# Optimization experiments

Hardware: AMD Instinct MI355X
Metric: run time of the kernel (lower is better)

## Reference

```python
import jax, jax.numpy as jnp
import numpy as np

B, S = 32, 128          # batch, seq_len
C, K = 256, 128         # num_concept, dim_k (== dim_e == dim_correct)
DC = 128                # dim_correct
NQ, NIT, NUT = 10000, 1024, 1024


def _xavier(k, shape):
    fan_out, fan_in = shape[0], shape[1]
    bound = float(np.sqrt(6.0 / (fan_in + fan_out)))
    return jax.random.uniform(k, shape, jnp.float32, -bound, bound)


def setup_inputs() -> dict:
    key = jax.random.key(0)
    ks = jax.random.split(key, 16)
    question_seq = jax.random.randint(ks[0], (B, S), 0, NQ + 1)
    interval_time_seq = jax.random.randint(ks[1], (B, S), 0, NIT + 1)
    use_time_seq = jax.random.randint(ks[2], (B, S), 0, NUT + 1)
    correct_seq = jnp.round(jax.random.uniform(ks[3], (B, S))).astype(jnp.float32)
    E_q = _xavier(ks[4], (NQ + 1, K))
    E_it = _xavier(ks[5], (NIT + 1, K))
    E_ut = _xavier(ks[6], (NUT + 1, K))
    q_matrix = (jax.random.uniform(ks[7], (NQ + 1, C)) < 0.03).astype(jnp.float32)
    h0 = _xavier(ks[8], (C, K))  # xavier init of the initial concept memory
    W1 = _xavier(ks[9], (K, K + K + DC)); b1 = jnp.zeros((K,), jnp.float32)
    W2 = _xavier(ks[10], (K, 4 * K));     b2 = jnp.zeros((K,), jnp.float32)
    W3 = _xavier(ks[11], (K, 4 * K));     b3 = jnp.zeros((K,), jnp.float32)
    W4 = _xavier(ks[12], (K, 3 * K));     b4 = jnp.zeros((K,), jnp.float32)
    W5 = _xavier(ks[13], (K, 2 * K));     b5 = jnp.zeros((K,), jnp.float32)
    return dict(question_seq=question_seq, interval_time_seq=interval_time_seq,
                use_time_seq=use_time_seq, correct_seq=correct_seq,
                E_q=E_q, E_it=E_it, E_ut=E_ut, q_matrix=q_matrix, h0=h0,
                W1=W1, b1=b1, W2=W2, b2=b2, W3=W3, b3=b3,
                W4=W4, b4=b4, W5=W5, b5=b5)


def _forward(question_seq, interval_time_seq, use_time_seq, correct_seq,
             E_q, E_it, E_ut, q_matrix, h0,
             W1, b1, W2, b2, W3, b3, W4, b4, W5, b5):
    bsz, slen = question_seq.shape
    dim_k = h0.shape[1]
    dim_c = W1.shape[1] - 2 * dim_k

    q_emb = E_q[question_seq]            # [B,S,K]
    it_emb = E_it[interval_time_seq]     # [B,S,K]
    ut_emb = E_ut[use_time_seq]          # [B,S,K]
    c_emb = jnp.broadcast_to(correct_seq[..., None], (bsz, slen, dim_c))
    all_learning = jnp.concatenate([q_emb, ut_emb, c_emb], -1) @ W1.T + b1  # [B,S,K]
    qe = q_matrix[question_seq]          # [B,S,C]

    h_pre0 = jnp.tile(h0[None], (bsz, 1, 1))                     # [B,C,K]
    h_tilde0 = jnp.einsum('bc,bck->bk', qe[:, 0], h_pre0)        # q_e @ h at t=0
    learning0 = jnp.zeros((bsz, dim_k), all_learning.dtype)

    # split linear_4 weight over its (h_pre, LG, it) concat blocks
    W4h, W4l, W4i = W4[:, :dim_k], W4[:, dim_k:2 * dim_k], W4[:, 2 * dim_k:]

    # time-major per-step inputs for t = 0 .. S-2
    xs = (jnp.swapaxes(it_emb[:, :-1], 0, 1),
          jnp.swapaxes(all_learning[:, :-1], 0, 1),
          jnp.swapaxes(qe[:, :-1], 0, 1),
          jnp.swapaxes(qe[:, 1:], 0, 1),
          jnp.swapaxes(q_emb[:, 1:], 0, 1))

    def step(carry, x):
        h_pre, h_tilde_pre, learning_pre = carry
        it, learning, qe_t, qe_n, qemb_n = x
        cat = jnp.concatenate([learning_pre, it, learning, h_tilde_pre], -1)  # [B,4K]
        learning_gain = jnp.tanh(cat @ W2.T + b2)
        gamma_l = jax.nn.sigmoid(cat @ W3.T + b3)
        LG = gamma_l * (learning_gain + 1.0) * 0.5                 # [B,K]
        LG_tilde = qe_t[:, :, None] * LG[:, None, :]               # [B,C,K] outer write
        gamma_f = jax.nn.sigmoid(jnp.einsum('bck,jk->bcj', h_pre, W4h)
                                 + (LG @ W4l.T + it @ W4i.T + b4)[:, None, :])
        h = LG_tilde + gamma_f * h_pre                             # [B,C,K]
        h_tilde = jnp.einsum('bc,bck->bk', qe_n, h)                # read for t+1
        y = jax.nn.sigmoid(jnp.concatenate([qemb_n, h_tilde], -1) @ W5.T + b5).sum(-1) / dim_k
        return (h, h_tilde, learning), y

    _, ys = jax.lax.scan(step, (h_pre0, h_tilde0, learning0), xs)  # ys: [S-1,B]
    pred = jnp.concatenate([jnp.zeros((bsz, 1), ys.dtype), ys.T], axis=1)
    return pred


def reference(question_seq, interval_time_seq, use_time_seq, correct_seq,
              E_q, E_it, E_ut, q_matrix, h0,
              W1, b1, W2, b2, W3, b3, W4, b4, W5, b5):
    return _forward(question_seq, interval_time_seq, use_time_seq, correct_seq,
                    E_q, E_it, E_ut, q_matrix, h0,
                    W1, b1, W2, b2, W3, b3, W4, b4, W5, b5)
```

## Files before the change

### kernel.cpp

```cpp
#include <hip/hip_runtime.h>
#include <hip/hip_bf16.h>


typedef __bf16 bf16x8 __attribute__((ext_vector_type(8)));
typedef __bf16 bf16x4 __attribute__((ext_vector_type(4)));
typedef float f32x4 __attribute__((ext_vector_type(4)));

#define HROW 136
#define HBUF (256*HROW)

__device__ __forceinline__ float sigmf(float x){
  return __builtin_amdgcn_rcpf(1.0f + __expf(-x));
}

__device__ __forceinline__ bf16x8 cvt8(float4 a, float4 b){
  bf16x8 r;
  r[0]=(__bf16)a.x; r[1]=(__bf16)a.y; r[2]=(__bf16)a.z; r[3]=(__bf16)a.w;
  r[4]=(__bf16)b.x; r[5]=(__bf16)b.y; r[6]=(__bf16)b.z; r[7]=(__bf16)b.w;
  return r;
}

__device__ __forceinline__ void mk_hilo(float4 a, float4 b, bf16x8& hi, bf16x8& lo){
  float v[8] = {a.x,a.y,a.z,a.w,b.x,b.y,b.z,b.w};
  #pragma unroll
  for (int i = 0; i < 8; i++){
    __bf16 h = (__bf16)v[i];
    hi[i] = h;
    lo[i] = (__bf16)(v[i] - (float)h);
  }
}

__device__ __forceinline__ f32x4 mfma16(bf16x8 a, bf16x8 b, f32x4 c){
  return __builtin_amdgcn_mfma_f32_16x16x32_bf16(a, b, c, 0, 0, 0);
}

__device__ __forceinline__ void red16(f32x4& r){
  #pragma unroll
  for (int m = 1; m < 16; m <<= 1){
    r[0] += __shfl_xor(r[0], m);
    r[1] += __shfl_xor(r[1], m);
    r[2] += __shfl_xor(r[2], m);
    r[3] += __shfl_xor(r[3], m);
  }
}

__global__ __launch_bounds__(256) void k1_al(
    const int* __restrict__ qseq, const int* __restrict__ utseq,
    const float* __restrict__ corr,
    const float* __restrict__ Eq, const float* __restrict__ Eut,
    const float* __restrict__ W1, const float* __restrict__ b1,
    const float* __restrict__ W5, const float* __restrict__ b5,
    float* __restrict__ AL, float* __restrict__ pre5)
{
  __shared__ __bf16 inA[64*256];
  __shared__ float corrs[64];
  __shared__ float b1s[128], b5s[128], rsp[256];
  const int tid = threadIdx.x, blk = blockIdx.x;
  if (tid < 128){ b1s[tid]=b1[tid]; b5s[tid]=b5[tid]; }
  {
    int j = tid & 127, hf = tid >> 7;
    const float* p = W1 + j*384 + 256 + hf*64;
    float s = 0.f;
    for (int i = 0; i < 64; i++) s += p[i];
    rsp[tid] = s;
  }
  {
    int r = tid >> 2, seg = tid & 3;
    int R = blk*64 + r;
    int qi = qseq[R], ui = utseq[R];
    if (seg == 0) corrs[r] = corr[R];
    for (int i = 0; i < 64; i++){
      int col = seg*64 + i;
      float v = (col < 128) ? Eq[qi*128 + col] : Eut[ui*128 + (col-128)];
      inA[((r*256 + col) ^ ((r&7)<<3))] = (__bf16)v;
    }
  }
  __syncthreads();
  const int w = tid >> 6, lane = tid & 63;
  const int la = lane & 15, g = lane >> 4;
  const int rbase = w*16;
  bf16x8 af[8];
  #pragma unroll
  for (int kt = 0; kt < 8; kt++){
    int idx = ((rbase+la)*256 + kt*32 + g*8) ^ ((la&7)<<3);
    af[kt] = *(const bf16x8*)&inA[idx];
  }
  for (int jt = 0; jt < 8; jt++){
    f32x4 acc = {0.f,0.f,0.f,0.f};
    const float* Wb = W1 + (jt*16+la)*384;
    #pragma unroll
    for (int kt = 0; kt < 8; kt++){
      const float* p = Wb + kt*32 + g*8;
      acc = mfma16(af[kt], cvt8(*(const float4*)p, *(const float4*)(p+4)), acc);
    }
    int j = jt*16 + la;
    float rsj = rsp[j] + rsp[j+128];
    #pragma unroll
    for (int rr = 0; rr < 4; rr++){
      int row = rbase + g*4 + rr;
      int R = blk*64 + row;
      AL[R*128 + j] = acc[rr] + b1s[j] + corrs[row]*rsj;
    }
  }
  for (int jt = 0; jt < 8; jt++){
    f32x4 acc = {0.f,0.f,0.f,0.f};
    const float* Wb = W5 + (jt*16+la)*256;
    #pragma unroll
    for (int kt = 0; kt < 4; kt++){
      const float* p = Wb + kt*32 + g*8;
      acc = mfma16(af[kt], cvt8(*(const float4*)p, *(const float4*)(p+4)), acc);
    }
    int j = jt*16 + la;
    #pragma unroll
    for (int rr = 0; rr < 4; rr++){
      int row = rbase + g*4 + rr;
      int R = blk*64 + row;
      pre5[R*128 + j] = acc[rr] + b5s[j];
    }
  }
}

__global__ __launch_bounds__(256) void k2_pre(
    const int* __restrict__ itseq, const float* __restrict__ Eit,
    const float* __restrict__ AL,
    const float* __restrict__ W2, const float* __restrict__ W3,
    const float* __restrict__ W4,
    const float* __restrict__ b2, const float* __restrict__ b3,
    const float* __restrict__ b4,
    float* __restrict__ pre23, float* __restrict__ pre4)
{
  __shared__ __bf16 inA[64*384];
  __shared__ int obase[64];
  __shared__ float b2s[128], b3s[128], b4s[128];
  const int tid = threadIdx.x, blk = blockIdx.x;
  if (tid < 128){ b2s[tid]=b2[tid]; b3s[tid]=b3[tid]; b4s[tid]=b4[tid]; }
  {
    int r = tid >> 2, seg = tid & 3;
    int R = blk*64 + r;
    bool valid = (R < 4064);
    int b_ = R / 127, tau = R % 127;
    if (seg == 0) obase[r] = valid ? (b_*127 + tau) : -1;
    int itv = valid ? itseq[b_*128 + tau] : 0;
    for (int i = 0; i < 96; i++){
      int col = seg*96 + i;
      float v = 0.f;
      if (valid){
        if (col < 128)      v = (tau > 0) ? AL[(b_*128 + tau-1)*128 + col] : 0.f;
        else if (col < 256) v = Eit[itv*128 + (col-128)];
        else                v = AL[(b_*128 + tau)*128 + (col-256)];
      }
      inA[((r*384 + col) ^ ((r&7)<<3))] = (__bf16)v;
    }
  }
  __syncthreads();
  const int w = tid >> 6, lane = tid & 63;
  const int la = lane & 15, g = lane >> 4;
  const int rbase = w*16;
  bf16x8 af[12];
  #pragma unroll
  for (int kt = 0; kt < 12; kt++){
    int idx = ((rbase+la)*384 + kt*32 + g*8) ^ ((la&7)<<3);
    af[kt] = *(const bf16x8*)&inA[idx];
  }
  for (int jt = 0; jt < 16; jt++){
    f32x4 acc = {0.f,0.f,0.f,0.f};
    int j = jt*16 + la;
    const float* Wb = (j < 128) ? (W2 + j*512) : (W3 + (j-128)*512);
    #pragma unroll
    for (int kt = 0; kt < 12; kt++){
      const float* p = Wb + kt*32 + g*8;
      acc = mfma16(af[kt], cvt8(*(const float4*)p, *(const float4*)(p+4)), acc);
    }
    float bias = (j < 128) ? b2s[j] : b3s[j-128];
    #pragma unroll
    for (int rr = 0; rr < 4; rr++){
      int row = rbase + g*4 + rr;
      int ob = obase[row];
      if (ob >= 0) pre23[ob*256 + j] = acc[rr] + bias;
    }
  }
  for (int jt = 0; jt < 8; jt++){
    f32x4 acc = {0.f,0.f,0.f,0.f};
    int j = jt*16 + la;
    const float* Wb = W4 + j*384 + 256;
    #pragma unroll
    for (int kk = 0; kk < 4; kk++){
      const float* p = Wb + kk*32 + g*8;
      acc = mfma16(af[4+kk], cvt8(*(const float4*)p, *(const float4*)(p+4)), acc);
    }
    #pragma unroll
    for (int rr = 0; rr < 4; rr++){
      int row = rbase + g*4 + rr;
      int ob = obase[row];
      if (ob >= 0) pre4[ob*128 + j] = acc[rr] + b4s[j];
    }
  }
}

#define SCAN_LDS_BYTES (37184*4)

__global__ __launch_bounds__(512, 2) void lpkt_scan(
    const float* __restrict__ qmat, const int* __restrict__ qseq,
    const float* __restrict__ h0,
    const float* __restrict__ W2, const float* __restrict__ W3,
    const float* __restrict__ W4,
    const float* __restrict__ pre23, const float* __restrict__ pre4,
    float* __restrict__ hist)
{
  extern __shared__ float lds[];
  __bf16* hB   = (__bf16*)lds;
  float*  htb0 = lds + 34816;
  float*  htb1 = lds + 35072;
  float*  LGb  = lds + 35328;
  __bf16* LGh  = (__bf16*)(lds + 35456);
  float*  qeb  = lds + 35520;
  float*  p23L = lds + 36288;
  float*  p4L  = lds + 36800;
  int*    qsl  = (int*)(lds + 37056);

  const int tid  = threadIdx.x;
  const int b    = blockIdx.x;
  const int lane = tid & 63;
  const int w    = tid >> 6;
  const int la   = lane & 15, g = lane >> 4;
  const int jq   = w & 3;
  const int ch   = w >> 2;

  bf16x8 af[2][4];
  bf16x8 af4l[2][4];
  #pragma unroll
  for (int jj = 0; jj < 2; jj++){
    #pragma unroll
    for (int kt = 0; kt < 4; kt++){
      const float* ph = W4 + ((jq*2+jj)*16+la)*384 + kt*32 + g*8;
      const float* pl = W4 + ((jq*2+jj)*16+la)*384 + 128 + kt*32 + g*8;
      af[jj][kt]   = cvt8(*(const float4*)ph, *(const float4*)(ph+4));
      af4l[jj][kt] = cvt8(*(const float4*)pl, *(const float4*)(pl+4));
    }
  }
  bf16x8 af23[2][4];
  #pragma unroll
  for (int kt = 0; kt < 4; kt++){
    const float* p2 = W2 + (w*16+la)*512 + 384 + kt*32 + g*8;
    const float* p3 = W3 + (w*16+la)*512 + 384 + kt*32 + g*8;
    af23[0][kt] = cvt8(*(const float4*)p2, *(const float4*)(p2+4));
    af23[1][kt] = cvt8(*(const float4*)p3, *(const float4*)(p3+4));
  }

  int rb[8], wb[8];
  #pragma unroll
  for (int cg = 0; cg < 8; cg++){
    const int c_ = ch*128 + cg*16 + la;
    rb[cg] = c_*HROW + g*8;
    wb[cg] = c_*HROW + jq*32 + g*4;
  }

  if (tid < 128) qsl[tid] = qseq[b*128 + tid];
  __syncthreads();
  const float* pre23b = pre23 + b*127*256;
  const float* pre4b  = pre4  + b*127*128;
  if (tid < 64)       *(float4*)&qeb[tid*4] = *(const float4*)(qmat + (size_t)qsl[0]*256 + tid*4);
  else if (tid < 128) *(float4*)&qeb[256 + (tid-64)*4] = *(const float4*)(qmat + (size_t)qsl[1]*256 + (tid-64)*4);
  else if (tid < 192) *(float4*)&p23L[(tid-128)*4] = *(const float4*)(pre23b + (tid-128)*4);
  else if (tid < 224) *(float4*)&p4L[(tid-192)*4]  = *(const float4*)(pre4b  + (tid-192)*4);

  float4 hreg[8][2];
  #pragma unroll
  for (int cg = 0; cg < 8; cg++){
    const int c_ = ch*128 + cg*16 + la;
    #pragma unroll
    for (int jj = 0; jj < 2; jj++){
      const int k0 = (jq*2+jj)*16 + g*4;
      float4 v = *(const float4*)(h0 + c_*128 + k0);
      hreg[cg][jj] = v;
      bf16x4 hb; hb[0]=(__bf16)v.x; hb[1]=(__bf16)v.y; hb[2]=(__bf16)v.z; hb[3]=(__bf16)v.w;
      *(bf16x4*)&hB[wb[cg] + jj*16] = hb;
    }
  }
  __syncthreads();
  {
    f32x4 r0 = {0.f,0.f,0.f,0.f}, r1 = {0.f,0.f,0.f,0.f};
    #pragma unroll
    for (int cg = 0; cg < 8; cg++){
      const int c_ = ch*128 + cg*16 + la;
      float q = qeb[c_];
      float4 h0v = hreg[cg][0], h1v = hreg[cg][1];
      r0[0] += q*h0v.x; r0[1] += q*h0v.y; r0[2] += q*h0v.z; r0[3] += q*h0v.w;
      r1[0] += q*h1v.x; r1[1] += q*h1v.y; r1[2] += q*h1v.z; r1[3] += q*h1v.w;
    }
    red16(r0); red16(r1);
    if (la == 0){
      float4 s0 = {r0[0],r0[1],r0[2],r0[3]};
      float4 s1 = {r1[0],r1[1],r1[2],r1[3]};
      *(float4*)&htb0[ch*128 + jq*32 + g*4]      = s0;
      *(float4*)&htb0[ch*128 + jq*32 + 16 + g*4] = s1;
    }
  }
  __syncthreads();

  int i0 = 0, i1 = 1, i2 = 2;

  for (int tau = 0; tau < 127; tau++){
    float* htc = (tau & 1) ? htb1 : htb0;
    float* htn = (tau & 1) ? htb0 : htb1;
    float* qec = qeb + i0*256;
    float* qen = qeb + i1*256;
    float* qep = qeb + i2*256;
    const float* p23c = p23L + (tau & 1)*256;
    const float* p4c  = p4L  + (tau & 1)*128;
    const int roff = (tau & 1) ? HBUF : 0;
    const int woff = (tau & 1) ? 0 : HBUF;

    {
      bf16x8 xh[4], xl[4];
      #pragma unroll
      for (int kt = 0; kt < 4; kt++){
        int k0 = kt*32 + g*8;
        float4 a0 = *(const float4*)&htc[k0];
        float4 a1 = *(const float4*)&htc[k0+4];
        float4 b0 = *(const float4*)&htc[128 + k0];
        float4 b1v = *(const float4*)&htc[128 + k0+4];
        a0.x += b0.x; a0.y += b0.y; a0.z += b0.z; a0.w += b0.w;
        a1.x += b1v.x; a1.y += b1v.y; a1.z += b1v.z; a1.w += b1v.w;
        mk_hilo(a0, a1, xh[kt], xl[kt]);
      }
      f32x4 aLh = {0.f,0.f,0.f,0.f}, aLl = {0.f,0.f,0.f,0.f};
      f32x4 aGh = {0.f,0.f,0.f,0.f}, aGl = {0.f,0.f,0.f,0.f};
      #pragma unroll
      for (int kt = 0; kt < 4; kt++){
        aLh = mfma16(af23[0][kt], xh[kt], aLh);
        aLl = mfma16(af23[0][kt], xl[kt], aLl);
        aGh = mfma16(af23[1][kt], xh[kt], aGh);
        aGl = mfma16(af23[1][kt], xl[kt], aGl);
      }
      float4 lp4 = *(const float4*)&p23c[w*16 + g*4];
      float4 gp4 = *(const float4*)&p23c[128 + w*16 + g*4];
      float4 LG4;
      LG4.x = sigmf(aGh[0]+aGl[0]+gp4.x) * sigmf(2.f*(aLh[0]+aLl[0]+lp4.x));
      LG4.y = sigmf(aGh[1]+aGl[1]+gp4.y) * sigmf(2.f*(aLh[1]+aLl[1]+lp4.y));
      LG4.z = sigmf(aGh[2]+aGl[2]+gp4.z) * sigmf(2.f*(aLh[2]+aLl[2]+lp4.z));
      LG4.w = sigmf(aGh[3]+aGl[3]+gp4.w) * sigmf(2.f*(aLh[3]+aLl[3]+lp4.w));
      if (la == 0){
        *(float4*)&LGb[w*16 + g*4] = LG4;
        bf16x4 lgp;
        lgp[0]=(__bf16)LG4.x; lgp[1]=(__bf16)LG4.y;
        lgp[2]=(__bf16)LG4.z; lgp[3]=(__bf16)LG4.w;
        *(bf16x4*)&LGh[w*16 + g*4] = lgp;
      }
    }
    __syncthreads();

    float4 pf23, pf4, pfqe;
    const bool dopf = (tau < 126);
    const bool do23 = dopf && (tid < 64);
    const bool do4  = dopf && (tid >= 64) && (tid < 96);
    const bool doqe = dopf && (tid >= 448);
    if (do23) pf23 = *(const float4*)(pre23b + (tau+1)*256 + tid*4);
    if (do4)  pf4  = *(const float4*)(pre4b  + (tau+1)*128 + (tid-64)*4);
    if (doqe) pfqe = *(const float4*)(qmat + (size_t)qsl[tau+2]*256 + (tid-448)*4);
    if (tau > 0 && tid >= 96 && tid < 128){
      int i = (tid - 96)*4;
      float4 v0 = *(const float4*)&htc[i];
      float4 v1 = *(const float4*)&htc[128 + i];
      float4 v = {v0.x+v1.x, v0.y+v1.y, v0.z+v1.z, v0.w+v1.w};
      *(float4*)(hist + ((size_t)b*127 + (tau-1))*128 + i) = v;
    }

    float4 z4[2];
    {
      bf16x8 lh[4];
      #pragma unroll
      for (int kt = 0; kt < 4; kt++)
        lh[kt] = *(const bf16x8*)&LGh[kt*32 + g*8];
      #pragma unroll
      for (int jj = 0; jj < 2; jj++){
        f32x4 az = {0.f,0.f,0.f,0.f};
        #pragma unroll
        for (int kt = 0; kt < 4; kt++)
          az = mfma16(af4l[jj][kt], lh[kt], az);
        float4 zp = *(const float4*)&p4c[(jq*2+jj)*16 + g*4];
        z4[jj].x = az[0]+zp.x; z4[jj].y = az[1]+zp.y;
        z4[jj].z = az[2]+zp.z; z4[jj].w = az[3]+zp.w;
      }
    }
    float4 lg4[2];
    #pragma unroll
    for (int jj = 0; jj < 2; jj++)
      lg4[jj] = *(const float4*)&LGb[(jq*2+jj)*16 + g*4];

    bf16x8 bA[4], bB[4];
    {
      const int base = rb[0] + roff;
      #pragma unroll
      for (int kt = 0; kt < 4; kt++) bA[kt] = *(const bf16x8*)&hB[base + kt*32];
    }
    f32x4 r0 = {0.f,0.f,0.f,0.f}, r1 = {0.f,0.f,0.f,0.f};
    #pragma unroll
    for (int cg = 0; cg < 8; cg++){
      const bf16x8* cur = (cg & 1) ? bB : bA;
      bf16x8*       nxt = (cg & 1) ? bA : bB;
      if (cg < 7){
        const int base = rb[cg+1] + roff;
        #pragma unroll
        for (int kt = 0; kt < 4; kt++) nxt[kt] = *(const bf16x8*)&hB[base + kt*32];
      }
      const int c_ = ch*128 + cg*16 + la;
      const float qe_t = qec[c_], qe_n = qen[c_];
      const int wbase = wb[cg] + woff;
      #pragma unroll
      for (int jj = 0; jj < 2; jj++){
        f32x4 acc = {0.f,0.f,0.f,0.f};
        #pragma unroll
        for (int kt = 0; kt < 4; kt++)
          acc = mfma16(af[jj][kt], cur[kt], acc);
        float4 hp = hreg[cg][jj];
        float4 hn;
        hn.x = qe_t*lg4[jj].x + sigmf(acc[0] + z4[jj].x)*hp.x;
        hn.y = qe_t*lg4[jj].y + sigmf(acc[1] + z4[jj].y)*hp.y;
        hn.z = qe_t*lg4[jj].z + sigmf(acc[2] + z4[jj].z)*hp.z;
        hn.w = qe_t*lg4[jj].w + sigmf(acc[3] + z4[jj].w)*hp.w;
        hreg[cg][jj] = hn;
        bf16x4 hb; hb[0]=(__bf16)hn.x; hb[1]=(__bf16)hn.y; hb[2]=(__bf16)hn.z; hb[3]=(__bf16)hn.w;
        *(bf16x4*)&hB[wbase + jj*16] = hb;
        f32x4& r = (jj == 0) ? r0 : r1;
        r[0] += qe_n*hn.x; r[1] += qe_n*hn.y;
        r[2] += qe_n*hn.z; r[3] += qe_n*hn.w;
      }
    }
    red16(r0); red16(r1);
    if (la == 0){
      float4 s0 = {r0[0],r0[1],r0[2],r0[3]};
      float4 s1 = {r1[0],r1[1],r1[2],r1[3]};
      *(float4*)&htn[ch*128 + jq*32 + g*4]      = s0;
      *(float4*)&htn[ch*128 + jq*32 + 16 + g*4] = s1;
    }
    if (do23) *(float4*)&p23L[((tau+1)&1)*256 + tid*4] = pf23;
    if (do4)  *(float4*)&p4L[((tau+1)&1)*128 + (tid-64)*4] = pf4;
    if (doqe) *(float4*)&qep[(tid-448)*4] = pfqe;
    __syncthreads();
    int t_ = i0; i0 = i1; i1 = i2; i2 = t_;
  }

  if (tid < 32){
    int i = tid*4;
    float4 v0 = *(const float4*)&htb1[i];
    float4 v1 = *(const float4*)&htb1[128 + i];
    float4 v = {v0.x+v1.x, v0.y+v1.y, v0.z+v1.z, v0.w+v1.w};
    *(float4*)(hist + ((size_t)b*127 + 126)*128 + i) = v;
  }
}

__global__ __launch_bounds__(128) void k4_y(
    const float* __restrict__ hist, const float* __restrict__ pre5,
    const float* __restrict__ W5, float* __restrict__ out)
{
  const int R = blockIdx.x;
  const int s = R & 127, b = R >> 7;
  const int j = threadIdx.x;
  __shared__ float xs[128];
  __shared__ float partial[2];
  if (s == 0){ if (j == 0) out[R] = 0.f; return; }
  xs[j] = hist[((size_t)b*127 + (s-1))*128 + j];
  __syncthreads();
  const float* wr = W5 + j*256 + 128;
  float acc = pre5[(size_t)R*128 + j];
  #pragma unroll
  for (int k = 0; k < 128; k += 4){
    float4 wv = *(const float4*)&wr[k];
    float4 xv = *(const float4*)&xs[k];
    acc += wv.x*xv.x + wv.y*xv.y + wv.z*xv.z + wv.w*xv.w;
  }
  float v = sigmf(acc);
  #pragma unroll
  for (int m = 1; m < 64; m <<= 1) v += __shfl_xor(v, m);
  if ((j & 63) == 0) partial[j >> 6] = v;
  __syncthreads();
  if (j == 0) out[R] = (partial[0] + partial[1]) * (1.f/128.f);
}

extern "C" void kernel_launch(void* const* d_in, const int* in_sizes, int n_in,
                              void* d_out, int out_size, void* d_ws, size_t ws_size,
                              hipStream_t stream) {
  const int*   qseq  = (const int*)  d_in[0];
  const int*   itseq = (const int*)  d_in[1];
  const int*   utseq = (const int*)  d_in[2];
  const float* corr  = (const float*)d_in[3];
  const float* Eq    = (const float*)d_in[4];
  const float* Eit   = (const float*)d_in[5];
  const float* Eut   = (const float*)d_in[6];
  const float* qmat  = (const float*)d_in[7];
  const float* h0    = (const float*)d_in[8];
  const float* W1    = (const float*)d_in[9];
  const float* b1    = (const float*)d_in[10];
  const float* W2    = (const float*)d_in[11];
  const float* b2    = (const float*)d_in[12];
  const float* W3    = (const float*)d_in[13];
  const float* b3    = (const float*)d_in[14];
  const float* W4    = (const float*)d_in[15];
  const float* b4    = (const float*)d_in[16];
  const float* W5    = (const float*)d_in[17];
  const float* b5    = (const float*)d_in[18];
  float* out = (float*)d_out;

  float* ws    = (float*)d_ws;
  float* AL    = ws;
  float* hist  = ws;
  float* pre5  = ws + 524288;
  float* pre23 = ws + 1048576;
  float* pre4  = ws + 2088960;

  (void)hipFuncSetAttribute(reinterpret_cast<const void*>(&lpkt_scan),
                            hipFuncAttributeMaxDynamicSharedMemorySize,
                            SCAN_LDS_BYTES);

  hipLaunchKernelGGL(k1_al, dim3(64), dim3(256), 0, stream,
                     qseq, utseq, corr, Eq, Eut, W1, b1, W5, b5, AL, pre5);
  hipLaunchKernelGGL(k2_pre, dim3(64), dim3(256), 0, stream,
                     itseq, Eit, AL, W2, W3, W4, b2, b3, b4, pre23, pre4);
  hipLaunchKernelGGL(lpkt_scan, dim3(32), dim3(512), SCAN_LDS_BYTES, stream,
                     qmat, qseq, h0, W2, W3, W4, pre23, pre4, hist);
  hipLaunchKernelGGL(k4_y, dim3(4096), dim3(128), 0, stream,
                     hist, pre5, W5, out);
}
```

Baseline: 867.4 us.

## Swizzle concept memory LDS layout and use DPP row reductions

```diff
diff --git a/kernel.cpp b/kernel.cpp
--- a/kernel.cpp
+++ b/kernel.cpp
@@ -6,8 +6,7 @@
 typedef __bf16 bf16x4 __attribute__((ext_vector_type(4)));
 typedef float f32x4 __attribute__((ext_vector_type(4)));
 
-#define HROW 136
-#define HBUF (256*HROW)
+#define HBUF 32768
 
 __device__ __forceinline__ float sigmf(float x){
   return __builtin_amdgcn_rcpf(1.0f + __expf(-x));
@@ -34,14 +33,24 @@
   return __builtin_amdgcn_mfma_f32_16x16x32_bf16(a, b, c, 0, 0, 0);
 }
 
+__device__ __forceinline__ float dpp_sum16(float v){
+  int x;
+  x = __builtin_amdgcn_update_dpp(0, __builtin_bit_cast(int, v), 0x111, 0xf, 0xf, true);
+  v += __builtin_bit_cast(float, x);
+  x = __builtin_amdgcn_update_dpp(0, __builtin_bit_cast(int, v), 0x112, 0xf, 0xf, true);
+  v += __builtin_bit_cast(float, x);
+  x = __builtin_amdgcn_update_dpp(0, __builtin_bit_cast(int, v), 0x114, 0xf, 0xf, true);
+  v += __builtin_bit_cast(float, x);
+  x = __builtin_amdgcn_update_dpp(0, __builtin_bit_cast(int, v), 0x118, 0xf, 0xf, true);
+  v += __builtin_bit_cast(float, x);
+  return v;
+}
+
 __device__ __forceinline__ void red16(f32x4& r){
-  #pragma unroll
-  for (int m = 1; m < 16; m <<= 1){
-    r[0] += __shfl_xor(r[0], m);
-    r[1] += __shfl_xor(r[1], m);
-    r[2] += __shfl_xor(r[2], m);
-    r[3] += __shfl_xor(r[3], m);
-  }
+  r[0] = dpp_sum16(r[0]);
+  r[1] = dpp_sum16(r[1]);
+  r[2] = dpp_sum16(r[2]);
+  r[3] = dpp_sum16(r[3]);
 }
 
 __global__ __launch_bounds__(256) void k1_al(
@@ -197,7 +206,7 @@
   }
 }
 
-#define SCAN_LDS_BYTES (37184*4)
+#define SCAN_LDS_BYTES (35136*4)
 
 __global__ __launch_bounds__(512, 2) void lpkt_scan(
     const float* __restrict__ qmat, const int* __restrict__ qseq,
@@ -209,14 +218,14 @@
 {
   extern __shared__ float lds[];
   __bf16* hB   = (__bf16*)lds;
-  float*  htb0 = lds + 34816;
-  float*  htb1 = lds + 35072;
-  float*  LGb  = lds + 35328;
-  __bf16* LGh  = (__bf16*)(lds + 35456);
-  float*  qeb  = lds + 35520;
-  float*  p23L = lds + 36288;
-  float*  p4L  = lds + 36800;
-  int*    qsl  = (int*)(lds + 37056);
+  float*  htb0 = lds + 32768;
+  float*  htb1 = lds + 33024;
+  float*  LGb  = lds + 33280;
+  __bf16* LGh  = (__bf16*)(lds + 33408);
+  float*  qeb  = lds + 33472;
+  float*  p23L = lds + 34240;
+  float*  p4L  = lds + 34752;
+  int*    qsl  = (int*)(lds + 35008);
 
   const int tid  = threadIdx.x;
   const int b    = blockIdx.x;
@@ -250,9 +259,9 @@
   int rb[8], wb[8];
   #pragma unroll
   for (int cg = 0; cg < 8; cg++){
-    const int c_ = ch*128 + cg*16 + la;
-    rb[cg] = c_*HROW + g*8;
-    wb[cg] = c_*HROW + jq*32 + g*4;
+    const int cblk = ch*8 + cg;
+    rb[cg] = cblk*2048 + g*128 + la*8;
+    wb[cg] = cblk*2048 + jq*512 + (g>>1)*128 + la*8 + (g&1)*4;
   }
 
   if (tid < 128) qsl[tid] = qseq[b*128 + tid];
@@ -274,7 +283,7 @@
       float4 v = *(const float4*)(h0 + c_*128 + k0);
       hreg[cg][jj] = v;
       bf16x4 hb; hb[0]=(__bf16)v.x; hb[1]=(__bf16)v.y; hb[2]=(__bf16)v.z; hb[3]=(__bf16)v.w;
-      *(bf16x4*)&hB[wb[cg] + jj*16] = hb;
+      *(bf16x4*)&hB[wb[cg] + jj*256] = hb;
     }
   }
   __syncthreads();
@@ -289,7 +298,7 @@
       r1[0] += q*h1v.x; r1[1] += q*h1v.y; r1[2] += q*h1v.z; r1[3] += q*h1v.w;
     }
     red16(r0); red16(r1);
-    if (la == 0){
+    if (la == 15){
       float4 s0 = {r0[0],r0[1],r0[2],r0[3]};
       float4 s1 = {r1[0],r1[1],r1[2],r1[3]};
       *(float4*)&htb0[ch*128 + jq*32 + g*4]      = s0;
@@ -392,7 +401,7 @@
     {
       const int base = rb[0] + roff;
       #pragma unroll
-      for (int kt = 0; kt < 4; kt++) bA[kt] = *(const bf16x8*)&hB[base + kt*32];
+      for (int kt = 0; kt < 4; kt++) bA[kt] = *(const bf16x8*)&hB[base + kt*512];
     }
     f32x4 r0 = {0.f,0.f,0.f,0.f}, r1 = {0.f,0.f,0.f,0.f};
     #pragma unroll
@@ -402,7 +411,7 @@
       if (cg < 7){
         const int base = rb[cg+1] + roff;
         #pragma unroll
-        for (int kt = 0; kt < 4; kt++) nxt[kt] = *(const bf16x8*)&hB[base + kt*32];
+        for (int kt = 0; kt < 4; kt++) nxt[kt] = *(const bf16x8*)&hB[base + kt*512];
       }
       const int c_ = ch*128 + cg*16 + la;
       const float qe_t = qec[c_], qe_n = qen[c_];
@@ -421,14 +430,14 @@
         hn.w = qe_t*lg4[jj].w + sigmf(acc[3] + z4[jj].w)*hp.w;
         hreg[cg][jj] = hn;
         bf16x4 hb; hb[0]=(__bf16)hn.x; hb[1]=(__bf16)hn.y; hb[2]=(__bf16)hn.z; hb[3]=(__bf16)hn.w;
-        *(bf16x4*)&hB[wbase + jj*16] = hb;
+        *(bf16x4*)&hB[wbase + jj*256] = hb;
         f32x4& r = (jj == 0) ? r0 : r1;
         r[0] += qe_n*hn.x; r[1] += qe_n*hn.y;
         r[2] += qe_n*hn.z; r[3] += qe_n*hn.w;
       }
     }
     red16(r0); red16(r1);
-    if (la == 0){
+    if (la == 15){
       float4 s0 = {r0[0],r0[1],r0[2],r0[3]};
       float4 s1 = {r1[0],r1[1],r1[2],r1[3]};
       *(float4*)&htn[ch*128 + jq*32 + g*4]      = s0;
```

After: 821.8 us, median of 2. 1.06x faster.
